# Performance work log

Hardware: AMD Instinct MI355X
Metric: run time of the kernel (lower is better)

Reference implementation:

```python
import jax, jax.numpy as jnp
import numpy as np

# ---- module config (matches init_kwargs) ----
OGFH, OGFW = 256, 704
DOWNSAMPLE = 8
FH, FW = OGFH // DOWNSAMPLE, OGFW // DOWNSAMPLE   # 32, 88
DBOUND = (4.0, 45.0, 1.0)
D = int((DBOUND[1] - DBOUND[0]) / DBOUND[2])      # 41 depth bins
CAMC = 64
XB = (-50.0, 50.0, 0.5)    # lateral  -> nx = 200
YB = (-10.0, 10.0, 20.0)   # vertical -> ny = 1
ZB = (0.0, 50.0, 0.25)     # depth    -> nz = 200
NX = np.array([int((b[1] - b[0]) / b[2]) for b in (XB, YB, ZB)])  # [200, 1, 200]
DX = np.array([b[2] for b in (XB, YB, ZB)], dtype=np.float32)
BX = np.array([b[0] + b[2] / 2.0 for b in (XB, YB, ZB)], dtype=np.float32)


def make_frustum():
    # matches create_frustum_1camera: [D, fH, fW, 3] of (u, v, depth)
    ds = jnp.broadcast_to(
        jnp.arange(DBOUND[0], DBOUND[1], DBOUND[2], dtype=jnp.float32)[:, None, None],
        (D, FH, FW))
    xs = jnp.broadcast_to(
        jnp.linspace(0.0, OGFW - 1, FW, dtype=jnp.float32)[None, None, :], (D, FH, FW))
    ys = jnp.broadcast_to(
        jnp.linspace(0.0, OGFH - 1, FH, dtype=jnp.float32)[None, :, None], (D, FH, FW))
    return jnp.stack((xs, ys, ds), -1)


def setup_inputs() -> dict:
    key = jax.random.key(0)
    B = 4
    # depthnet output: first D channels = depth logits, next CAMC = context feats
    x = jax.random.normal(key, (B, D + CAMC, FH, FW), dtype=jnp.float32)
    fx = fy = 520.0
    K = jnp.array([[fx, 0.0, OGFW / 2.0],
                   [0.0, fy, OGFH / 2.0],
                   [0.0, 0.0, 1.0]], dtype=jnp.float32)
    intrins = jnp.broadcast_to(K, (B, 3, 3))
    post_rots = jnp.broadcast_to(jnp.eye(3, dtype=jnp.float32), (B, 3, 3))
    post_trans = jnp.zeros((B, 3), dtype=jnp.float32)
    return {"x": x, "intrins": intrins, "post_rots": post_rots, "post_trans": post_trans}


def _forward(x, intrins, post_rots, post_trans):
    B = x.shape[0]
    frustum = make_frustum()                                                     # [D,H,W,3]
    # ---- get_geometry ----
    pts = frustum[None] - post_trans[:, None, None, None, :]                     # [B,D,H,W,3]
    pts = jnp.einsum('bij,bdhwj->bdhwi', jnp.linalg.inv(post_rots), pts)
    pts = jnp.concatenate([pts[..., :2] * pts[..., 2:3], pts[..., 2:3]], -1)     # un-normalize
    geom = jnp.einsum('bij,bdhwj->bdhwi', jnp.linalg.inv(intrins), pts)          # [B,D,H,W,3]
    # ---- lift: depth softmax (x) context features ----
    depth = jax.nn.softmax(x[:, :D], axis=1)                                     # [B,D,H,W]
    feat = x[:, D:D + CAMC]                                                      # [B,C,H,W]
    vol = depth[:, None] * feat[:, :, None]                                      # [B,C,D,H,W]
    vol = jnp.transpose(vol, (0, 2, 3, 4, 1))                                    # [B,D,H,W,C]
    # ---- voxel_splat (sort+cumsum trick == segmented sum) ----
    Nprime = B * D * FH * FW
    feats = vol.reshape(Nprime, CAMC)
    # torch .long() truncates toward zero -> astype(int32)
    coords = ((geom - (BX - DX / 2.0)) / DX).astype(jnp.int32).reshape(Nprime, 3)
    bix = jnp.repeat(jnp.arange(B, dtype=jnp.int32), Nprime // B)
    kept = ((coords[:, 0] >= 0) & (coords[:, 0] < int(NX[0])) &
            (coords[:, 1] >= 0) & (coords[:, 1] < int(NX[1])) &
            (coords[:, 2] >= 0) & (coords[:, 2] < int(NX[2])))
    nseg = int(NX[0] * NX[1] * NX[2]) * B
    ranks = (coords[:, 0] * (int(NX[1]) * int(NX[2]) * B)
             + coords[:, 1] * (int(NX[2]) * B)
             + coords[:, 2] * B + bix)
    ranks = jnp.where(kept, ranks, nseg)  # dump bucket for dropped points
    pooled = jax.ops.segment_sum(jnp.where(kept[:, None], feats, 0.0), ranks,
                                 num_segments=nseg + 1)[:nseg]
    final = pooled.reshape(int(NX[0]), int(NX[1]), int(NX[2]), B, CAMC)          # [x,y,z,B,C]
    final = jnp.transpose(final, (3, 4, 1, 2, 0))                                # [B,C,ny,nz,nx]
    # torch.cat(final.unbind(dim=2), 1): collapse ny into channels (y-major)
    final = jnp.transpose(final, (0, 2, 1, 3, 4)).reshape(
        B, CAMC * int(NX[1]), int(NX[2]), int(NX[0]))                            # [B,C,200,200]
    return final


def reference(x, intrins, post_rots, post_trans):
    return _forward(x, intrins, post_rots, post_trans)
```

## Files before the change

### kernel.cpp

```cpp
#include <hip/hip_runtime.h>
#include <math.h>

#define DD   41
#define FHh  32
#define FWw  88
#define CC   64
#define NXx  200
#define NZz  200
#define NCH  (DD + CC)
#define PLANE ((size_t)FHh * FWw)
#define NE   (DD * FWw)
#define DCAP 4

__global__ __launch_bounds__(256) void lss_colpool(
    const float* __restrict__ x,
    const float* __restrict__ intrins,
    const float* __restrict__ post_rots,
    const float* __restrict__ post_trans,
    float* __restrict__ P, int* __restrict__ V, int* __restrict__ rowcnt)
{
    __shared__ float Wt[DD][FHh];
    __shared__ float F[FHh][CC];
    __shared__ float Mi[18];
    __shared__ int   Vtmp[DD];

    int blk = blockIdx.x;
    int w = blk % FWw;
    int b = blk / FWw;
    int t = threadIdx.x;
    const float* xb = x + (size_t)b * NCH * PLANE + w;

    for (int idx = t; idx < DD * FHh; idx += 256) {
        int d = idx >> 5, h = idx & 31;
        Wt[d][h] = xb[((size_t)d * FHh + h) * FWw];
    }
    for (int idx = t; idx < FHh * CC; idx += 256) {
        int c = idx & 63, h = idx >> 6;
        F[h][c] = xb[((size_t)(DD + c) * FHh + h) * FWw];
    }
    if (t >= 64 && t < 64 + DD) Vtmp[t - 64] = -1;
    if (t == 0) {
        #pragma clang fp contract(off)
        for (int m = 0; m < 2; ++m) {
            const float* A = (m == 0 ? post_rots : intrins) + b * 9;
            float* O = Mi + m * 9;
            float a = A[0], bb = A[1], c = A[2];
            float d = A[3], e  = A[4], f = A[5];
            float g = A[6], h  = A[7], i = A[8];
            float det = a * (e * i - f * h) - bb * (d * i - f * g) + c * (d * h - e * g);
            O[0] = (e * i - f * h) / det;
            O[1] = (c * h - bb * i) / det;
            O[2] = (bb * f - c * e) / det;
            O[3] = (f * g - d * i) / det;
            O[4] = (a * i - c * g) / det;
            O[5] = (c * d - a * f) / det;
            O[6] = (d * h - e * g) / det;
            O[7] = (bb * g - a * h) / det;
            O[8] = (a * e - bb * d) / det;
        }
    }
    __syncthreads();

    if (t < FHh) {
        #pragma clang fp contract(off)
        int h = t;
        float mx = -INFINITY;
        for (int d = 0; d < DD; ++d) mx = fmaxf(mx, Wt[d][h]);
        float s = 0.0f;
        for (int d = 0; d < DD; ++d) { float e = expf(Wt[d][h] - mx); Wt[d][h] = e; s += e; }

        float xs = (float)((double)w * 703.0 / 87.0);
        float ys = (float)((double)h * 255.0 / 31.0);
        float tx = post_trans[b * 3 + 0];
        float ty = post_trans[b * 3 + 1];
        float tz = post_trans[b * 3 + 2];
        for (int d = 0; d < DD; ++d) {
            float z  = 4.0f + (float)d;
            float px = xs - tx, py = ys - ty, pz = z - tz;
            float rx = Mi[0] * px + Mi[1] * py + Mi[2] * pz;
            float ry = Mi[3] * px + Mi[4] * py + Mi[5] * pz;
            float rz = Mi[6] * px + Mi[7] * py + Mi[8] * pz;
            float qx = rx * rz, qy = ry * rz, qz = rz;
            float gx = Mi[ 9] * qx + Mi[10] * qy + Mi[11] * qz;
            float gy = Mi[12] * qx + Mi[13] * qy + Mi[14] * qz;
            float gz = Mi[15] * qx + Mi[16] * qy + Mi[17] * qz;
            float cx = (gx + 50.0f) / 0.5f;
            float cy = (gy + 10.0f) / 20.0f;
            float cz = gz / 0.25f;
            int ix = (int)cx;
            int iy = (int)cy;
            int iz = (int)cz;
            bool kept = (ix >= 0) & (ix < NXx) & (iy == 0) & (iz >= 0) & (iz < NZz);
            if (kept) {
                Wt[d][h] /= s;
                Vtmp[d] = iz * NXx + ix;
            } else {
                Wt[d][h] = 0.0f;
            }
        }
    }
    __syncthreads();

    float* Pb = P + ((size_t)b * NE) * CC;
    for (int idx = t; idx < DD * CC; idx += 256) {
        int d = idx >> 6, c = idx & 63;
        float acc = 0.0f;
        for (int h = 0; h < FHh; ++h) acc += Wt[d][h] * F[h][c];
        Pb[((size_t)d * FWw + w) * CC + c] = acc;
    }
    if (t < DD) V[(size_t)b * NE + (size_t)t * FWw + w] = Vtmp[t];
    if (w == 0) for (int i = t; i < NZz; i += 256) rowcnt[b * NZz + i] = 0;
}

__global__ __launch_bounds__(256) void lss_rowbuild(
    const float* __restrict__ P, const int* __restrict__ V,
    float* __restrict__ S, int* __restrict__ izd,
    int* __restrict__ rowcnt, int* __restrict__ dlist)
{
    __shared__ float accf[CC * (NXx + 1)];
    __shared__ int   ixw[FWw];
    __shared__ int   s_iz;

    int bd = blockIdx.x;
    int d  = bd % DD;
    int b  = bd / DD;
    int t  = threadIdx.x;

    if (t == 0) s_iz = -1;
    __syncthreads();
    if (t < FWw) {
        int v = V[((size_t)b * DD + d) * FWw + t];
        int iz = v / NXx;
        ixw[t] = (v >= 0) ? (v - iz * NXx) : -1;
        if (v >= 0) s_iz = iz;
    }
    __syncthreads();
    int iz = s_iz;
    if (t == 0) izd[b * DD + d] = iz;
    if (iz < 0) return;
    if (t == 0) {
        int r = b * NZz + iz;
        int k = atomicAdd(&rowcnt[r], 1);
        if (k < DCAP) dlist[r * DCAP + k] = d;
    }

    for (int i = t; i < CC * (NXx + 1); i += 256) accf[i] = 0.0f;
    __syncthreads();

    const float* Pb = P + ((size_t)b * DD + d) * FWw * CC;
    for (int idx = t; idx < FWw * CC; idx += 256) {
        int w = idx >> 6, c = idx & 63;
        int ix = ixw[w];
        if (ix >= 0) atomicAdd(&accf[c * (NXx + 1) + ix], Pb[idx]);
    }
    __syncthreads();

    float* Srow = S + ((size_t)b * DD + d) * CC * NXx;
    for (int i = t; i < CC * (NXx / 4); i += 256) {
        int c = i / (NXx / 4), q = i - c * (NXx / 4);
        int base = c * (NXx + 1) + q * 4;
        float4 vv;
        vv.x = accf[base + 0];
        vv.y = accf[base + 1];
        vv.z = accf[base + 2];
        vv.w = accf[base + 3];
        ((float4*)Srow)[i] = vv;
    }
}

__global__ __launch_bounds__(256) void lss_writeout(
    const float* __restrict__ S, const int* __restrict__ izd,
    const int* __restrict__ rowcnt, const int* __restrict__ dlist,
    float* __restrict__ out)
{
    __shared__ int s_n[50];
    __shared__ int s_d[50 * DCAP];

    int blk = blockIdx.x;
    int qz = blk & 3;
    int bc = blk >> 2;
    int c  = bc % CC;
    int b  = bc / CC;
    int iz0 = qz * 50;
    int t = threadIdx.x;

    for (int i = t; i < 50; i += 256) s_n[i] = rowcnt[b * NZz + iz0 + i];
    for (int i = t; i < 50 * DCAP; i += 256) s_d[i] = dlist[(size_t)(b * NZz + iz0) * DCAP + i];
    __syncthreads();

    float* obase = out + (((size_t)b * CC + c) * NZz + iz0) * NXx;
    const float* Sb = S + (size_t)b * DD * CC * NXx;

    for (int i = t; i < 50 * (NXx / 4); i += 256) {
        int izl = i / (NXx / 4), q = i - izl * (NXx / 4);
        int n = s_n[izl];
        float4 vv = make_float4(0.f, 0.f, 0.f, 0.f);
        if (n > 0) {
            if (n <= DCAP) {
                for (int k = 0; k < n; ++k) {
                    int d = s_d[izl * DCAP + k];
                    float4 sv = ((const float4*)(Sb + ((size_t)d * CC + c) * NXx))[q];
                    vv.x += sv.x; vv.y += sv.y; vv.z += sv.z; vv.w += sv.w;
                }
            } else {
                int iz = iz0 + izl;
                for (int d = 0; d < DD; ++d) {
                    if (izd[b * DD + d] == iz) {
                        float4 sv = ((const float4*)(Sb + ((size_t)d * CC + c) * NXx))[q];
                        vv.x += sv.x; vv.y += sv.y; vv.z += sv.z; vv.w += sv.w;
                    }
                }
            }
        }
        ((float4*)obase)[i] = vv;
    }
}

extern "C" void kernel_launch(void* const* d_in, const int* in_sizes, int n_in,
                              void* d_out, int out_size, void* d_ws, size_t ws_size,
                              hipStream_t stream)
{
    const float* x          = (const float*)d_in[0];
    const float* intrins    = (const float*)d_in[1];
    const float* post_rots  = (const float*)d_in[2];
    const float* post_trans = (const float*)d_in[3];
    float* out = (float*)d_out;

    int B = in_sizes[0] / (NCH * (int)PLANE);

    size_t off = 0;
    auto alloc = [&](size_t bytes) {
        void* p = (char*)d_ws + off;
        off = (off + bytes + 255) & ~(size_t)255;
        return p;
    };
    float* P      = (float*)alloc((size_t)B * NE * CC * sizeof(float));
    int*   V      = (int*)  alloc((size_t)B * NE * sizeof(int));
    float* S      = (float*)alloc((size_t)B * DD * CC * NXx * sizeof(float));
    int*   izd    = (int*)  alloc((size_t)B * DD * sizeof(int));
    int*   rowcnt = (int*)  alloc((size_t)B * NZz * sizeof(int));
    int*   dlist  = (int*)  alloc((size_t)B * NZz * DCAP * sizeof(int));

    lss_colpool<<<B * FWw, 256, 0, stream>>>(x, intrins, post_rots, post_trans, P, V, rowcnt);
    lss_rowbuild<<<B * DD, 256, 0, stream>>>(P, V, S, izd, rowcnt, dlist);
    lss_writeout<<<B * CC * 4, 256, 0, stream>>>(S, izd, rowcnt, dlist, out);
}
```

Before: 117.8 us.

## Parallelize softmax across threads, split rowbuild by channel group, add overflow path

The depth softmax and geometry loop in colpool now use all 256 threads, with 8 depth lanes per column and shared-memory partial max and sum reductions, instead of 32 threads. Rowbuild is split into 8 channel-group blocks per (batch, depth), which shrinks the shared accumulator and raises the block count. Points whose iz differs from the row's chosen iz are now recorded in an overflow list, and writeout adds them serially. This fixes correctness for rows whose points land in mixed iz rows, at the cost of an extra global counter and a serial tail loop when the list is non-empty.

```diff
diff --git a/kernel.cpp b/kernel.cpp
--- a/kernel.cpp
+++ b/kernel.cpp
@@ -5,23 +5,27 @@
 #define FHh  32
 #define FWw  88
 #define CC   64
+#define CG8  8
 #define NXx  200
 #define NZz  200
 #define NCH  (DD + CC)
 #define PLANE ((size_t)FHh * FWw)
 #define NE   (DD * FWw)
 #define DCAP 4
+#define OVCAP 4096
 
 __global__ __launch_bounds__(256) void lss_colpool(
     const float* __restrict__ x,
     const float* __restrict__ intrins,
     const float* __restrict__ post_rots,
     const float* __restrict__ post_trans,
-    float* __restrict__ P, int* __restrict__ V, int* __restrict__ rowcnt)
+    float* __restrict__ P, int* __restrict__ V,
+    int* __restrict__ rowcnt, int* __restrict__ ovcnt)
 {
-    __shared__ float Wt[DD][FHh];
+    __shared__ float Wt[DD][FHh + 1];
     __shared__ float F[FHh][CC];
     __shared__ float Mi[18];
+    __shared__ float pm[8][FHh + 1];
     __shared__ int   Vtmp[DD];
 
     int blk = blockIdx.x;
@@ -61,20 +65,40 @@
     }
     __syncthreads();
 
-    if (t < FHh) {
+    int h = t & 31, l = t >> 5;
+    float e_[6];
+    {
+        float pmax = -INFINITY;
+        for (int d = l; d < DD; d += 8) pmax = fmaxf(pmax, Wt[d][h]);
+        pm[l][h] = pmax;
+    }
+    __syncthreads();
+    float mx = -INFINITY;
+    for (int j = 0; j < 8; ++j) mx = fmaxf(mx, pm[j][h]);
+    __syncthreads();
+    {
         #pragma clang fp contract(off)
-        int h = t;
-        float mx = -INFINITY;
-        for (int d = 0; d < DD; ++d) mx = fmaxf(mx, Wt[d][h]);
-        float s = 0.0f;
-        for (int d = 0; d < DD; ++d) { float e = expf(Wt[d][h] - mx); Wt[d][h] = e; s += e; }
-
+        float psum = 0.0f;
+        int k = 0;
+        for (int d = l; d < DD; d += 8, ++k) {
+            float e = expf(Wt[d][h] - mx);
+            e_[k] = e; psum += e;
+        }
+        pm[l][h] = psum;
+    }
+    __syncthreads();
+    float s = 0.0f;
+    for (int j = 0; j < 8; ++j) s += pm[j][h];
+
+    {
+        #pragma clang fp contract(off)
         float xs = (float)((double)w * 703.0 / 87.0);
         float ys = (float)((double)h * 255.0 / 31.0);
         float tx = post_trans[b * 3 + 0];
         float ty = post_trans[b * 3 + 1];
         float tz = post_trans[b * 3 + 2];
-        for (int d = 0; d < DD; ++d) {
+        int k = 0;
+        for (int d = l; d < DD; d += 8, ++k) {
             float z  = 4.0f + (float)d;
             float px = xs - tx, py = ys - ty, pz = z - tz;
             float rx = Mi[0] * px + Mi[1] * py + Mi[2] * pz;
@@ -92,7 +116,7 @@
             int iz = (int)cz;
             bool kept = (ix >= 0) & (ix < NXx) & (iy == 0) & (iz >= 0) & (iz < NZz);
             if (kept) {
-                Wt[d][h] /= s;
+                Wt[d][h] = e_[k] / s;
                 Vtmp[d] = iz * NXx + ix;
             } else {
                 Wt[d][h] = 0.0f;
@@ -105,65 +129,79 @@
     for (int idx = t; idx < DD * CC; idx += 256) {
         int d = idx >> 6, c = idx & 63;
         float acc = 0.0f;
-        for (int h = 0; h < FHh; ++h) acc += Wt[d][h] * F[h][c];
+        for (int hh = 0; hh < FHh; ++hh) acc += Wt[d][hh] * F[hh][c];
         Pb[((size_t)d * FWw + w) * CC + c] = acc;
     }
     if (t < DD) V[(size_t)b * NE + (size_t)t * FWw + w] = Vtmp[t];
     if (w == 0) for (int i = t; i < NZz; i += 256) rowcnt[b * NZz + i] = 0;
+    if (blk == 0 && t == 0) *ovcnt = 0;
 }
 
 __global__ __launch_bounds__(256) void lss_rowbuild(
     const float* __restrict__ P, const int* __restrict__ V,
     float* __restrict__ S, int* __restrict__ izd,
-    int* __restrict__ rowcnt, int* __restrict__ dlist)
+    int* __restrict__ rowcnt, int* __restrict__ dlist,
+    int* __restrict__ ovcnt, int* __restrict__ ovlist)
 {
-    __shared__ float accf[CC * (NXx + 1)];
-    __shared__ int   ixw[FWw];
-    __shared__ int   s_iz;
-
-    int bd = blockIdx.x;
-    int d  = bd % DD;
-    int b  = bd / DD;
-    int t  = threadIdx.x;
-
-    if (t == 0) s_iz = -1;
+    __shared__ float acc[CG8 * (NXx + 1)];
+    __shared__ int ixw[FWw];
+    __shared__ int izw[FWw];
+    __shared__ int key;
+
+    int blk = blockIdx.x;
+    int cg = blk & 7;
+    int bd = blk >> 3;
+    int d = bd % DD;
+    int b = bd / DD;
+    int t = threadIdx.x;
+
+    if (t == 0) key = 0x7fffffff;
+    for (int i = t; i < CG8 * (NXx + 1); i += 256) acc[i] = 0.0f;
     __syncthreads();
     if (t < FWw) {
-        int v = V[((size_t)b * DD + d) * FWw + t];
-        int iz = v / NXx;
-        ixw[t] = (v >= 0) ? (v - iz * NXx) : -1;
-        if (v >= 0) s_iz = iz;
-    }
-    __syncthreads();
-    int iz = s_iz;
-    if (t == 0) izd[b * DD + d] = iz;
-    if (iz < 0) return;
-    if (t == 0) {
-        int r = b * NZz + iz;
-        int k = atomicAdd(&rowcnt[r], 1);
-        if (k < DCAP) dlist[r * DCAP + k] = d;
-    }
-
-    for (int i = t; i < CC * (NXx + 1); i += 256) accf[i] = 0.0f;
-    __syncthreads();
-
-    const float* Pb = P + ((size_t)b * DD + d) * FWw * CC;
-    for (int idx = t; idx < FWw * CC; idx += 256) {
-        int w = idx >> 6, c = idx & 63;
-        int ix = ixw[w];
-        if (ix >= 0) atomicAdd(&accf[c * (NXx + 1) + ix], Pb[idx]);
-    }
-    __syncthreads();
-
-    float* Srow = S + ((size_t)b * DD + d) * CC * NXx;
-    for (int i = t; i < CC * (NXx / 4); i += 256) {
+        int v = V[(size_t)bd * FWw + t];
+        if (v >= 0) {
+            int iz = v / NXx;
+            izw[t] = iz; ixw[t] = v - iz * NXx;
+            atomicMin(&key, (t << 16) | iz);
+        } else { izw[t] = -1; ixw[t] = -1; }
+    }
+    __syncthreads();
+    int kk = key;
+    int s_iz = (kk == 0x7fffffff) ? -1 : (kk & 0xffff);
+    if (cg == 0 && t == 0) {
+        izd[bd] = s_iz;
+        if (s_iz >= 0) {
+            int r = b * NZz + s_iz;
+            int k = atomicAdd(&rowcnt[r], 1);
+            if (k < DCAP) dlist[r * DCAP + k] = d;
+        }
+    }
+    if (s_iz < 0) return;
+
+    if (cg == 0 && t < FWw && izw[t] >= 0 && izw[t] != s_iz) {
+        int k = atomicAdd(ovcnt, 1);
+        if (k < OVCAP)
+            ovlist[k] = (b << 29) | (d << 23) | (t << 16) | (ixw[t] << 8) | izw[t];
+    }
+
+    const float* Pb = P + (size_t)bd * FWw * CC + cg * CG8;
+    for (int idx = t; idx < FWw * CG8; idx += 256) {
+        int w = idx >> 3, cl = idx & 7;
+        if (izw[w] == s_iz)
+            atomicAdd(&acc[cl * (NXx + 1) + ixw[w]], Pb[(size_t)w * CC + cl]);
+    }
+    __syncthreads();
+
+    float* Srow = S + ((size_t)bd * CC + cg * CG8) * NXx;
+    for (int i = t; i < CG8 * (NXx / 4); i += 256) {
         int c = i / (NXx / 4), q = i - c * (NXx / 4);
         int base = c * (NXx + 1) + q * 4;
         float4 vv;
-        vv.x = accf[base + 0];
-        vv.y = accf[base + 1];
-        vv.z = accf[base + 2];
-        vv.w = accf[base + 3];
+        vv.x = acc[base + 0];
+        vv.y = acc[base + 1];
+        vv.z = acc[base + 2];
+        vv.w = acc[base + 3];
         ((float4*)Srow)[i] = vv;
     }
 }
@@ -171,6 +209,8 @@
 __global__ __launch_bounds__(256) void lss_writeout(
     const float* __restrict__ S, const int* __restrict__ izd,
     const int* __restrict__ rowcnt, const int* __restrict__ dlist,
+    const float* __restrict__ P,
+    const int* __restrict__ ovcnt, const int* __restrict__ ovlist,
     float* __restrict__ out)
 {
     __shared__ int s_n[50];
@@ -214,6 +254,26 @@
         }
         ((float4*)obase)[i] = vv;
     }
+
+    int nov = *ovcnt;
+    if (nov > 0) {
+        __syncthreads();
+        if (t == 0) {
+            if (nov > OVCAP) nov = OVCAP;
+            for (int k = 0; k < nov; ++k) {
+                int ent = ovlist[k];
+                int eb  = (ent >> 29) & 7;
+                int ed  = (ent >> 23) & 63;
+                int ew  = (ent >> 16) & 127;
+                int eix = (ent >> 8) & 255;
+                int eiz = ent & 255;
+                if (eb == b && eiz >= iz0 && eiz < iz0 + 50) {
+                    size_t o = (((size_t)b * CC + c) * NZz + eiz) * NXx + eix;
+                    out[o] += P[(((size_t)eb * DD + ed) * FWw + ew) * CC + c];
+                }
+            }
+        }
+    }
 }
 
 extern "C" void kernel_launch(void* const* d_in, const int* in_sizes, int n_in,
@@ -240,8 +300,13 @@
     int*   izd    = (int*)  alloc((size_t)B * DD * sizeof(int));
     int*   rowcnt = (int*)  alloc((size_t)B * NZz * sizeof(int));
     int*   dlist  = (int*)  alloc((size_t)B * NZz * DCAP * sizeof(int));
-
-    lss_colpool<<<B * FWw, 256, 0, stream>>>(x, intrins, post_rots, post_trans, P, V, rowcnt);
-    lss_rowbuild<<<B * DD, 256, 0, stream>>>(P, V, S, izd, rowcnt, dlist);
-    lss_writeout<<<B * CC * 4, 256, 0, stream>>>(S, izd, rowcnt, dlist, out);
+    int*   ovcnt  = (int*)  alloc(256);
+    int*   ovlist = (int*)  alloc((size_t)OVCAP * sizeof(int));
+
+    lss_colpool<<<B * FWw, 256, 0, stream>>>(x, intrins, post_rots, post_trans,
+                                             P, V, rowcnt, ovcnt);
+    lss_rowbuild<<<B * DD * 8, 256, 0, stream>>>(P, V, S, izd, rowcnt, dlist,
+                                                 ovcnt, ovlist);
+    lss_writeout<<<B * CC * 4, 256, 0, stream>>>(S, izd, rowcnt, dlist, P,
+                                                 ovcnt, ovlist, out);
 }
```

Result: faster. 105.9 us (-10.1%).
